# Kernel optimization log

Hardware: AMD Instinct MI355X
Metric: run time of the kernel (lower is better)

## Reference

```python
import jax, jax.numpy as jnp
import numpy as np

NEG_SLOPE = 0.2

def gat_conv(x, src, dst, W, a_src, a_dst, b, num_nodes):
    # x: [N, in]; W: [in, H*F]; a_src/a_dst: [H, F]; b: [H*F]
    H, F = a_src.shape
    feat = (x @ W).reshape(-1, H, F)                 # [N, H, F]
    el = jnp.sum(feat * a_src, axis=-1)              # [N, H]
    er = jnp.sum(feat * a_dst, axis=-1)              # [N, H]
    e = jax.nn.leaky_relu(el[src] + er[dst], NEG_SLOPE)  # [E, H]
    # segment softmax over incoming edges of each dst node
    emax = jax.ops.segment_max(e, dst, num_segments=num_nodes)  # [N, H]
    ee = jnp.exp(e - emax[dst])
    denom = jax.ops.segment_sum(ee, dst, num_segments=num_nodes)  # [N, H]
    alpha = ee / denom[dst]                          # [E, H]
    msg = feat[src] * alpha[..., None]               # [E, H, F]
    out = jax.ops.segment_sum(msg, dst, num_segments=num_nodes)  # [N, H, F]
    return out + b.reshape(1, H, F)


def setup_inputs() -> dict:
    key = jax.random.key(0)
    ks = jax.random.split(key, 16)
    N, E = 50000, 800000
    IN, HID, OUT, H = 128, 32, 32, 4
    inp = {
        'features': jax.random.normal(ks[0], (N, IN), dtype=jnp.float32),
        'edge_src': jax.random.randint(ks[1], (E,), 0, N, dtype=jnp.int32),
        'edge_dst': jax.random.randint(ks[2], (E,), 0, N, dtype=jnp.int32),
        'W1': jax.random.normal(ks[3], (IN, H * HID), dtype=jnp.float32) * 0.1,
        'a1s': jax.random.normal(ks[4], (H, HID), dtype=jnp.float32) * 0.1,
        'a1d': jax.random.normal(ks[5], (H, HID), dtype=jnp.float32) * 0.1,
        'b1': jnp.zeros((H * HID,), dtype=jnp.float32),
        'W2': jax.random.normal(ks[6], (H * HID, H * HID), dtype=jnp.float32) * 0.1,
        'a2s': jax.random.normal(ks[7], (H, HID), dtype=jnp.float32) * 0.1,
        'a2d': jax.random.normal(ks[8], (H, HID), dtype=jnp.float32) * 0.1,
        'b2': jnp.zeros((H * HID,), dtype=jnp.float32),
        'W3': jax.random.normal(ks[9], (H * HID, OUT), dtype=jnp.float32) * 0.1,
        'a3s': jax.random.normal(ks[10], (1, OUT), dtype=jnp.float32) * 0.1,
        'a3d': jax.random.normal(ks[11], (1, OUT), dtype=jnp.float32) * 0.1,
        'b3': jnp.zeros((OUT,), dtype=jnp.float32),
    }
    return inp


def reference(features, edge_src, edge_dst, W1, a1s, a1d, b1, W2, a2s, a2d, b2, W3, a3s, a3d, b3):
    N = features.shape[0]
    # dropout=0.0 -> identity
    x = gat_conv(features, edge_src, edge_dst, W1, a1s, a1d, b1, N).reshape(N, -1)
    x = jax.nn.elu(x)
    x = gat_conv(x, edge_src, edge_dst, W2, a2s, a2d, b2, N).reshape(N, -1)
    x = jax.nn.elu(x)
    x = gat_conv(x, edge_src, edge_dst, W3, a3s, a3d, b3, N).mean(axis=1)  # [N, out]
    return x
```

## Files before the change

### kernel.cpp

```cpp
#include <hip/hip_runtime.h>
#include <hip/hip_fp16.h>

#define NEG_SLOPE 0.2f

typedef unsigned int uint;
typedef unsigned short ushort;
typedef __attribute__((ext_vector_type(8))) short bf16x8;
typedef __attribute__((ext_vector_type(4))) float f32x4;
typedef __attribute__((ext_vector_type(2))) float f32x2;

__device__ __forceinline__ uint pack_bf16x2(float a, float b) {
    uint ba = __float_as_uint(a);
    uint bb = __float_as_uint(b);
    uint ra = (ba + 0x7FFFu + ((ba >> 16) & 1u)) >> 16;
    uint rb = (bb + 0x7FFFu + ((bb >> 16) & 1u)) >> 16;
    return ra | (rb << 16);
}

__device__ __forceinline__ ushort bf16_rne(float v) {
    uint b = __float_as_uint(v);
    return (ushort)((b + 0x7FFFu + ((b >> 16) & 1u)) >> 16);
}

__device__ __forceinline__ f32x2 unpack2(uint u) {
    f32x2 r;
    r.x = __uint_as_float(u << 16);
    r.y = __uint_as_float(u & 0xFFFF0000u);
    return r;
}

__device__ __forceinline__ uint pack_sw(int s, float w) {
    return ((uint)s << 16) | (uint)__half_as_ushort(__float2half_rn(w));
}

__device__ __forceinline__ int sw_src(uint u) { return (int)(u >> 16); }
__device__ __forceinline__ float sw_w(uint u) {
    return __half2float(__ushort_as_half((ushort)(u & 0xFFFFu)));
}


__global__ void zero_ints(int* __restrict__ p, int n) {
    int i = blockIdx.x * 256 + threadIdx.x;
    if (i < n) p[i] = 0;
}

__global__ void hist_kernel(const int* __restrict__ dst, int* __restrict__ deg,
                            int* __restrict__ rank, int E) {
    int i = blockIdx.x * 256 + threadIdx.x;
    if (i < E) rank[i] = atomicAdd(&deg[dst[i]], 1);
}

#define SCAN_CH 2048

__global__ __launch_bounds__(256) void scan_blocksum(const int* __restrict__ deg,
                                                     int* __restrict__ bsum, int N) {
    int blk = blockIdx.x, t = threadIdx.x;
    int base = blk * SCAN_CH;
    int s = 0;
#pragma unroll
    for (int i = 0; i < SCAN_CH / 256; ++i) {
        int idx = base + t + i * 256;
        if (idx < N) s += deg[idx];
    }
#pragma unroll
    for (int off = 1; off < 64; off <<= 1) s += __shfl_xor(s, off);
    __shared__ int wt[4];
    if ((t & 63) == 0) wt[t >> 6] = s;
    __syncthreads();
    if (t == 0) bsum[blk] = wt[0] + wt[1] + wt[2] + wt[3];
}

__global__ void scan_bsum(const int* __restrict__ bsum, int* __restrict__ boff, int nb) {
    int t = threadIdx.x;
    int orig = (t < nb) ? bsum[t] : 0;
    int v = orig;
#pragma unroll
    for (int off = 1; off < 64; off <<= 1) {
        int u = __shfl_up(v, off);
        if (t >= off) v += u;
    }
    if (t < nb) boff[t] = v - orig;
}

__global__ __launch_bounds__(256) void scan_write(const int* __restrict__ deg,
                                                  const int* __restrict__ boff,
                                                  int* __restrict__ rowptr, int N) {
    int blk = blockIdx.x, t = threadIdx.x;
    int base = blk * SCAN_CH + t * 8;
    int v[8];
    int s = 0;
#pragma unroll
    for (int r = 0; r < 8; ++r) {
        int idx = base + r;
        v[r] = (idx < N) ? deg[idx] : 0;
        s += v[r];
    }
    int lane = t & 63, wid = t >> 6;
    int p = s;
#pragma unroll
    for (int off = 1; off < 64; off <<= 1) {
        int u = __shfl_up(p, off);
        if (lane >= off) p += u;
    }
    __shared__ int wtot[4];
    if (lane == 63) wtot[wid] = p;
    __syncthreads();
    int run = boff[blk];
    for (int w = 0; w < wid; ++w) run += wtot[w];
    run += p - s;
#pragma unroll
    for (int r = 0; r < 8; ++r) {
        int idx = base + r;
        if (idx < N) {
            rowptr[idx] = run;
            run += v[r];
            if (idx == N - 1) rowptr[N] = run;
        }
    }
}

__global__ void fill_kernel(const int* __restrict__ src, const int* __restrict__ dst,
                            const int* __restrict__ rowptr, const int* __restrict__ rank,
                            int* __restrict__ csrc, int E) {
    int i = blockIdx.x * 256 + threadIdx.x;
    if (i < E) {
        int d = dst[i];
        __builtin_nontemporal_store(src[i], csrc + rowptr[d] + rank[i]);
    }
}


__global__ __launch_bounds__(256) void cvt_bf16_kernel(const float* __restrict__ X,
                                                       ushort* __restrict__ Xb, int n8) {
    int i = blockIdx.x * 256 + threadIdx.x;
    if (i >= n8) return;
    const float4* xp = (const float4*)X + (size_t)i * 2;
    float4 v0 = xp[0], v1 = xp[1];
    uint4 q;
    q.x = pack_bf16x2(v0.x, v0.y);
    q.y = pack_bf16x2(v0.z, v0.w);
    q.z = pack_bf16x2(v1.x, v1.y);
    q.w = pack_bf16x2(v1.z, v1.w);
    ((uint4*)Xb)[i] = q;
}


template <int OUTF>
__global__ __launch_bounds__(256) void wpack_kernel(const float* __restrict__ W,
                                                    ushort* __restrict__ wfrag) {
    constexpr int TOT = (OUTF / 16) * 4 * 64;
    int idx = blockIdx.x * 256 + threadIdx.x;
    if (idx >= TOT) return;
    int lane = idx & 63;
    int kt = (idx >> 6) & 3;
    int ct = idx >> 8;
    int col = ct * 16 + (lane & 15);
    int k0 = kt * 32 + (lane >> 4) * 8;
    uint4 q;
    q.x = pack_bf16x2(W[(k0 + 0) * OUTF + col], W[(k0 + 1) * OUTF + col]);
    q.y = pack_bf16x2(W[(k0 + 2) * OUTF + col], W[(k0 + 3) * OUTF + col]);
    q.z = pack_bf16x2(W[(k0 + 4) * OUTF + col], W[(k0 + 5) * OUTF + col]);
    q.w = pack_bf16x2(W[(k0 + 6) * OUTF + col], W[(k0 + 7) * OUTF + col]);
    ((uint4*)wfrag)[idx] = q;
}


template <int OUTF>
__global__ __launch_bounds__(256) void gemm_mfma_kernel(const ushort* __restrict__ Xb,
                                                        const ushort* __restrict__ wfrag,
                                                        ushort* __restrict__ Yb,
                                                        const float* __restrict__ as_,
                                                        const float* __restrict__ ad_,
                                                        float* __restrict__ el,
                                                        float* __restrict__ er, int N) {
    constexpr int H = OUTF / 32;
    constexpr int NCT = OUTF / 16;
    int lane = threadIdx.x & 63;
    int wv = threadIdx.x >> 6;
    int r0 = blockIdx.x * 64 + wv * 16;
    if (r0 >= N) return;
    int lrow = lane & 15;
    int lk8 = lane >> 4;

    bf16x8 afrag[4];
    {
        int arow = min(r0 + lrow, N - 1);
        const ushort* xr = Xb + (size_t)arow * 128;
#pragma unroll
        for (int kt = 0; kt < 4; ++kt)
            afrag[kt] = *(const bf16x8*)(xr + kt * 32 + lk8 * 8);
    }

    float pel[H][4];
    float prr[H][4];
#pragma unroll
    for (int h = 0; h < H; ++h)
#pragma unroll
        for (int j = 0; j < 4; ++j) { pel[h][j] = 0.f; prr[h][j] = 0.f; }

    const bf16x8* wf = (const bf16x8*)wfrag;
#pragma unroll
    for (int ct = 0; ct < NCT; ++ct) {
        f32x4 acc = {0.f, 0.f, 0.f, 0.f};
#pragma unroll
        for (int kt = 0; kt < 4; ++kt) {
            bf16x8 b = wf[(ct * 4 + kt) * 64 + lane];
            acc = __builtin_amdgcn_mfma_f32_16x16x32_bf16(afrag[kt], b, acc, 0, 0, 0);
        }
        int col = ct * 16 + lrow;
        int h = (H == 1) ? 0 : (ct >> 1);
        float asc = as_[col], adc = ad_[col];
#pragma unroll
        for (int j = 0; j < 4; ++j) {
            int row = r0 + lk8 * 4 + j;
            float v = acc[j];
            if (row < N) Yb[(size_t)row * OUTF + col] = bf16_rne(v);
            pel[h][j] = fmaf(v, asc, pel[h][j]);
            prr[h][j] = fmaf(v, adc, prr[h][j]);
        }
    }

#pragma unroll
    for (int h = 0; h < H; ++h)
#pragma unroll
        for (int j = 0; j < 4; ++j) {
            float pe = pel[h][j], pr = prr[h][j];
#pragma unroll
            for (int off = 1; off < 16; off <<= 1) {
                pe += __shfl_xor(pe, off);
                pr += __shfl_xor(pr, off);
            }
            if (lrow == 0) {
                int row = r0 + lk8 * 4 + j;
                if (row < N) {
                    el[row * H + h] = pe;
                    er[row * H + h] = pr;
                }
            }
        }
}


template <bool DOELU>
__global__ __launch_bounds__(256) void agg4_kernel(const ushort* __restrict__ featb,
                                                   const float* __restrict__ el,
                                                   const float* __restrict__ er,
                                                   const int* __restrict__ rowptr,
                                                   const int* __restrict__ csrc,
                                                   const float* __restrict__ bias,
                                                   ushort* __restrict__ outb, int N) {
    int lane = threadIdx.x & 63;
    int node = blockIdx.x * 4 + (threadIdx.x >> 6);
    if (node >= N) return;
    int row0 = __builtin_amdgcn_readfirstlane(rowptr[node]);
    int row1 = __builtin_amdgcn_readfirstlane(rowptr[node + 1]);

    int qe = lane >> 2;
    int qh = lane & 3;
    float ern = er[node * 4 + qh];

    int g = lane >> 4;
    int li = lane & 15;
    int h = li >> 2;
    int ib = (g << 4) + (h << 2);

    float dacc = 0.f;
    f32x2 acc2[4];
#pragma unroll
    for (int r = 0; r < 4; ++r) acc2[r] = (f32x2){0.f, 0.f};

    for (int base = row0; base < row1; base += 16) {
        int e = base + qe;
        uint u = 0;
        if (e < row1) {
            int s = csrc[e];
            float tt = el[s * 4 + qh] + ern;
            tt = tt > 0.f ? tt : NEG_SLOPE * tt;
            float w = __expf(tt);
            dacc += w;
            u = pack_sw(s, w);
        }
        uint u0 = (uint)__builtin_amdgcn_ds_bpermute(ib, (int)u);
        uint u1 = (uint)__builtin_amdgcn_ds_bpermute(ib + 64, (int)u);
        uint u2 = (uint)__builtin_amdgcn_ds_bpermute(ib + 128, (int)u);
        uint u3 = (uint)__builtin_amdgcn_ds_bpermute(ib + 192, (int)u);
        uint4 U0 = *(const uint4*)(featb + (size_t)sw_src(u0) * 128 + li * 8);
        uint4 U1 = *(const uint4*)(featb + (size_t)sw_src(u1) * 128 + li * 8);
        uint4 U2 = *(const uint4*)(featb + (size_t)sw_src(u2) * 128 + li * 8);
        uint4 U3 = *(const uint4*)(featb + (size_t)sw_src(u3) * 128 + li * 8);
        float w0 = sw_w(u0), w1 = sw_w(u1), w2 = sw_w(u2), w3 = sw_w(u3);
        acc2[0] = unpack2(U0.x) * w0 + acc2[0];
        acc2[1] = unpack2(U0.y) * w0 + acc2[1];
        acc2[2] = unpack2(U0.z) * w0 + acc2[2];
        acc2[3] = unpack2(U0.w) * w0 + acc2[3];
        acc2[0] = unpack2(U1.x) * w1 + acc2[0];
        acc2[1] = unpack2(U1.y) * w1 + acc2[1];
        acc2[2] = unpack2(U1.z) * w1 + acc2[2];
        acc2[3] = unpack2(U1.w) * w1 + acc2[3];
        acc2[0] = unpack2(U2.x) * w2 + acc2[0];
        acc2[1] = unpack2(U2.y) * w2 + acc2[1];
        acc2[2] = unpack2(U2.z) * w2 + acc2[2];
        acc2[3] = unpack2(U2.w) * w2 + acc2[3];
        acc2[0] = unpack2(U3.x) * w3 + acc2[0];
        acc2[1] = unpack2(U3.y) * w3 + acc2[1];
        acc2[2] = unpack2(U3.z) * w3 + acc2[2];
        acc2[3] = unpack2(U3.w) * w3 + acc2[3];
    }

#pragma unroll
    for (int r = 0; r < 4; ++r) {
        acc2[r].x += __shfl_xor(acc2[r].x, 16);
        acc2[r].y += __shfl_xor(acc2[r].y, 16);
        acc2[r].x += __shfl_xor(acc2[r].x, 32);
        acc2[r].y += __shfl_xor(acc2[r].y, 32);
    }
#pragma unroll
    for (int off = 4; off < 64; off <<= 1) dacc += __shfl_xor(dacc, off);
    float d = __int_as_float(
        __builtin_amdgcn_ds_bpermute((li >> 2) << 2, __float_as_int(dacc)));

    if (lane < 16) {
        float inv = (row1 > row0) ? 1.f / d : 0.f;
        const float4* bv = (const float4*)bias + li * 2;
        float4 b0 = bv[0], b1 = bv[1];
        float o[8];
        o[0] = acc2[0].x * inv + b0.x;
        o[1] = acc2[0].y * inv + b0.y;
        o[2] = acc2[1].x * inv + b0.z;
        o[3] = acc2[1].y * inv + b0.w;
        o[4] = acc2[2].x * inv + b1.x;
        o[5] = acc2[2].y * inv + b1.y;
        o[6] = acc2[3].x * inv + b1.z;
        o[7] = acc2[3].y * inv + b1.w;
        if (DOELU) {
#pragma unroll
            for (int r = 0; r < 8; ++r) o[r] = o[r] > 0.f ? o[r] : __expf(o[r]) - 1.f;
        }
        uint4 q;
        q.x = pack_bf16x2(o[0], o[1]);
        q.y = pack_bf16x2(o[2], o[3]);
        q.z = pack_bf16x2(o[4], o[5]);
        q.w = pack_bf16x2(o[6], o[7]);
        *(uint4*)(outb + (size_t)node * 128 + li * 8) = q;
    }
}


__global__ __launch_bounds__(256) void agg1_kernel(const ushort* __restrict__ featb,
                                                   const float* __restrict__ el,
                                                   const float* __restrict__ er,
                                                   const int* __restrict__ rowptr,
                                                   const int* __restrict__ csrc,
                                                   const float* __restrict__ bias,
                                                   float* __restrict__ out, int N) {
    int lane = threadIdx.x & 63;
    int node = blockIdx.x * 4 + (threadIdx.x >> 6);
    if (node >= N) return;
    int row0 = __builtin_amdgcn_readfirstlane(rowptr[node]);
    int row1 = __builtin_amdgcn_readfirstlane(rowptr[node + 1]);

    float ern = er[node];
    int g = lane >> 3;
    int li = lane & 7;

    float dacc = 0.f;
    f32x2 acc2[2];
    acc2[0] = (f32x2){0.f, 0.f};
    acc2[1] = (f32x2){0.f, 0.f};

    for (int base = row0; base < row1; base += 64) {
        int e = base + lane;
        uint u = 0;
        if (e < row1) {
            int s = csrc[e];
            float t0 = el[s] + ern;
            t0 = t0 > 0.f ? t0 : NEG_SLOPE * t0;
            float w0 = __expf(t0);
            dacc += w0;
            u = pack_sw(s, w0);
        }
        int cnt = min(row1 - base, 64);
        int iters = (cnt + 7) >> 3;
        int it = 0;
        for (; it + 1 < iters; it += 2) {
            int idxA = ((it << 3) + g) << 2;
            int idxB = (((it + 1) << 3) + g) << 2;
            uint uA = (uint)__builtin_amdgcn_ds_bpermute(idxA, (int)u);
            uint uB = (uint)__builtin_amdgcn_ds_bpermute(idxB, (int)u);
            uint2 UA = *(const uint2*)(featb + (size_t)sw_src(uA) * 32 + li * 4);
            uint2 UB = *(const uint2*)(featb + (size_t)sw_src(uB) * 32 + li * 4);
            float wA = sw_w(uA), wB = sw_w(uB);
            acc2[0] = unpack2(UA.x) * wA + acc2[0];
            acc2[1] = unpack2(UA.y) * wA + acc2[1];
            acc2[0] = unpack2(UB.x) * wB + acc2[0];
            acc2[1] = unpack2(UB.y) * wB + acc2[1];
        }
        if (it < iters) {
            int idx = ((it << 3) + g) << 2;
            uint uS = (uint)__builtin_amdgcn_ds_bpermute(idx, (int)u);
            uint2 U = *(const uint2*)(featb + (size_t)sw_src(uS) * 32 + li * 4);
            float wS = sw_w(uS);
            acc2[0] = unpack2(U.x) * wS + acc2[0];
            acc2[1] = unpack2(U.y) * wS + acc2[1];
        }
    }

#pragma unroll
    for (int r = 0; r < 2; ++r) {
        acc2[r].x += __shfl_xor(acc2[r].x, 8);
        acc2[r].y += __shfl_xor(acc2[r].y, 8);
        acc2[r].x += __shfl_xor(acc2[r].x, 16);
        acc2[r].y += __shfl_xor(acc2[r].y, 16);
        acc2[r].x += __shfl_xor(acc2[r].x, 32);
        acc2[r].y += __shfl_xor(acc2[r].y, 32);
    }
#pragma unroll
    for (int off = 1; off < 64; off <<= 1) dacc += __shfl_xor(dacc, off);

    if (lane < 8) {
        float inv = (row1 > row0) ? 1.f / dacc : 0.f;
        float4 b0 = ((const float4*)bias)[lane];
        float4 q;
        q.x = acc2[0].x * inv + b0.x;
        q.y = acc2[0].y * inv + b0.y;
        q.z = acc2[1].x * inv + b0.z;
        q.w = acc2[1].y * inv + b0.w;
        ((float4*)(out + (size_t)node * 32))[lane] = q;
    }
}


extern "C" void kernel_launch(void* const* d_in, const int* in_sizes, int n_in,
                              void* d_out, int out_size, void* d_ws, size_t ws_size,
                              hipStream_t stream) {
    const float* features = (const float*)d_in[0];
    const int* esrc = (const int*)d_in[1];
    const int* edst = (const int*)d_in[2];
    const float* W1 = (const float*)d_in[3];
    const float* a1s = (const float*)d_in[4];
    const float* a1d = (const float*)d_in[5];
    const float* b1 = (const float*)d_in[6];
    const float* W2 = (const float*)d_in[7];
    const float* a2s = (const float*)d_in[8];
    const float* a2d = (const float*)d_in[9];
    const float* b2 = (const float*)d_in[10];
    const float* W3 = (const float*)d_in[11];
    const float* a3s = (const float*)d_in[12];
    const float* a3d = (const float*)d_in[13];
    const float* b3 = (const float*)d_in[14];

    int N = in_sizes[0] / 128;
    int E = in_sizes[1];
    int nb = (N + SCAN_CH - 1) / SCAN_CH;

    char* base = (char*)d_ws;
    size_t off = 0;
    auto nxt = [&](size_t bytes) {
        void* p = base + off;
        off += (bytes + 255) & ~(size_t)255;
        return p;
    };
    ushort* Xb = (ushort*)nxt((size_t)N * 128 * 2);
    ushort* Yb = (ushort*)nxt((size_t)N * 128 * 2);
    ushort* Bb = (ushort*)nxt((size_t)N * 128 * 2);
    ushort* Y3b = (ushort*)nxt((size_t)N * 32 * 2);
    float* el = (float*)nxt((size_t)N * 4 * 4);
    float* er = (float*)nxt((size_t)N * 4 * 4);
    int* deg = (int*)nxt((size_t)N * 4);
    int* rowptr = (int*)nxt((size_t)(N + 1) * 4);
    int* csrc = (int*)nxt((size_t)E * 4);
    int* rank = (int*)nxt((size_t)E * 4);
    int* bsum = (int*)nxt((size_t)(nb + 1) * 4);
    int* boff = (int*)nxt((size_t)(nb + 1) * 4);
    ushort* wf1 = (ushort*)nxt(16384 * 2);
    ushort* wf2 = (ushort*)nxt(16384 * 2);
    ushort* wf3 = (ushort*)nxt(4096 * 2);

    int gemm_grid = (N + 63) / 64;

    zero_ints<<<(N + 255) / 256, 256, 0, stream>>>(deg, N);
    hist_kernel<<<(E + 255) / 256, 256, 0, stream>>>(edst, deg, rank, E);
    cvt_bf16_kernel<<<(N * 16 + 255) / 256, 256, 0, stream>>>(features, Xb, N * 16);
    wpack_kernel<128><<<8, 256, 0, stream>>>(W1, wf1);
    wpack_kernel<128><<<8, 256, 0, stream>>>(W2, wf2);
    wpack_kernel<32><<<2, 256, 0, stream>>>(W3, wf3);
    scan_blocksum<<<nb, 256, 0, stream>>>(deg, bsum, N);
    scan_bsum<<<1, 64, 0, stream>>>(bsum, boff, nb);
    scan_write<<<nb, 256, 0, stream>>>(deg, boff, rowptr, N);
    fill_kernel<<<(E + 255) / 256, 256, 0, stream>>>(esrc, edst, rowptr, rank, csrc, E);

    gemm_mfma_kernel<128><<<gemm_grid, 256, 0, stream>>>(Xb, wf1, Yb, a1s, a1d, el, er, N);
    agg4_kernel<true><<<(N + 3) / 4, 256, 0, stream>>>(Yb, el, er, rowptr, csrc, b1, Bb, N);

    gemm_mfma_kernel<128><<<gemm_grid, 256, 0, stream>>>(Bb, wf2, Yb, a2s, a2d, el, er, N);
    agg4_kernel<true><<<(N + 3) / 4, 256, 0, stream>>>(Yb, el, er, rowptr, csrc, b2, Bb, N);

    gemm_mfma_kernel<32><<<gemm_grid, 256, 0, stream>>>(Bb, wf3, Y3b, a3s, a3d, el, er, N);
    agg1_kernel<<<(N + 3) / 4, 256, 0, stream>>>(Y3b, el, er, rowptr, csrc, b3,
                                                 (float*)d_out, N);
}
```

Measured before the change: 225.7 us.

## Merge prep kernels, use memset for degree zeroing, prefetch next edge in agg4

The bf16 feature conversion and the three weight-packing kernels become one prep kernel that dispatches on block index, and the degree-zeroing kernel becomes a hipMemsetAsync. Together these cut several small launches from the preprocessing chain. The agg4 aggregation loop now loads the next chunk's source index and el value before the current chunk's gathers and FMAs, hiding some of the dependent load latency. The prefetch keeps extra values live in registers and adds loads on the last iteration.

```diff
diff --git a/kernel.cpp b/kernel.cpp
--- a/kernel.cpp
+++ b/kernel.cpp
@@ -38,11 +38,6 @@
     return __half2float(__ushort_as_half((ushort)(u & 0xFFFFu)));
 }
 
-
-__global__ void zero_ints(int* __restrict__ p, int n) {
-    int i = blockIdx.x * 256 + threadIdx.x;
-    if (i < n) p[i] = 0;
-}
 
 __global__ void hist_kernel(const int* __restrict__ dst, int* __restrict__ deg,
                             int* __restrict__ rank, int E) {
@@ -130,26 +125,10 @@
 }
 
 
-__global__ __launch_bounds__(256) void cvt_bf16_kernel(const float* __restrict__ X,
-                                                       ushort* __restrict__ Xb, int n8) {
-    int i = blockIdx.x * 256 + threadIdx.x;
-    if (i >= n8) return;
-    const float4* xp = (const float4*)X + (size_t)i * 2;
-    float4 v0 = xp[0], v1 = xp[1];
-    uint4 q;
-    q.x = pack_bf16x2(v0.x, v0.y);
-    q.y = pack_bf16x2(v0.z, v0.w);
-    q.z = pack_bf16x2(v1.x, v1.y);
-    q.w = pack_bf16x2(v1.z, v1.w);
-    ((uint4*)Xb)[i] = q;
-}
-
-
 template <int OUTF>
-__global__ __launch_bounds__(256) void wpack_kernel(const float* __restrict__ W,
-                                                    ushort* __restrict__ wfrag) {
+__device__ __forceinline__ void wpack_body(const float* __restrict__ W,
+                                           ushort* __restrict__ wfrag, int idx) {
     constexpr int TOT = (OUTF / 16) * 4 * 64;
-    int idx = blockIdx.x * 256 + threadIdx.x;
     if (idx >= TOT) return;
     int lane = idx & 63;
     int kt = (idx >> 6) & 3;
@@ -162,6 +141,37 @@
     q.z = pack_bf16x2(W[(k0 + 4) * OUTF + col], W[(k0 + 5) * OUTF + col]);
     q.w = pack_bf16x2(W[(k0 + 6) * OUTF + col], W[(k0 + 7) * OUTF + col]);
     ((uint4*)wfrag)[idx] = q;
+}
+
+__global__ __launch_bounds__(256) void prep_kernel(const float* __restrict__ X,
+                                                   ushort* __restrict__ Xb, int n8,
+                                                   int cvtblocks,
+                                                   const float* __restrict__ W1,
+                                                   ushort* __restrict__ wf1,
+                                                   const float* __restrict__ W2,
+                                                   ushort* __restrict__ wf2,
+                                                   const float* __restrict__ W3,
+                                                   ushort* __restrict__ wf3) {
+    int b = blockIdx.x;
+    int t = threadIdx.x;
+    if (b < cvtblocks) {
+        int i = b * 256 + t;
+        if (i >= n8) return;
+        const float4* xp = (const float4*)X + (size_t)i * 2;
+        float4 v0 = xp[0], v1 = xp[1];
+        uint4 q;
+        q.x = pack_bf16x2(v0.x, v0.y);
+        q.y = pack_bf16x2(v0.z, v0.w);
+        q.z = pack_bf16x2(v1.x, v1.y);
+        q.w = pack_bf16x2(v1.z, v1.w);
+        ((uint4*)Xb)[i] = q;
+    } else if (b < cvtblocks + 8) {
+        wpack_body<128>(W1, wf1, (b - cvtblocks) * 256 + t);
+    } else if (b < cvtblocks + 16) {
+        wpack_body<128>(W2, wf2, (b - cvtblocks - 8) * 256 + t);
+    } else {
+        wpack_body<32>(W3, wf3, (b - cvtblocks - 16) * 256 + t);
+    }
 }
 
 
@@ -269,17 +279,25 @@
 #pragma unroll
     for (int r = 0; r < 4; ++r) acc2[r] = (f32x2){0.f, 0.f};
 
+    int e0 = row0 + qe;
+    bool v = e0 < row1;
+    int s = v ? csrc[e0] : 0;
+    float elv = v ? el[s * 4 + qh] : 0.f;
+
     for (int base = row0; base < row1; base += 16) {
-        int e = base + qe;
         uint u = 0;
-        if (e < row1) {
-            int s = csrc[e];
-            float tt = el[s * 4 + qh] + ern;
+        if (v) {
+            float tt = elv + ern;
             tt = tt > 0.f ? tt : NEG_SLOPE * tt;
             float w = __expf(tt);
             dacc += w;
             u = pack_sw(s, w);
         }
+        int en = base + 16 + qe;
+        bool vn = en < row1;
+        int sn = vn ? csrc[en] : 0;
+        float elvn = vn ? el[sn * 4 + qh] : 0.f;
+
         uint u0 = (uint)__builtin_amdgcn_ds_bpermute(ib, (int)u);
         uint u1 = (uint)__builtin_amdgcn_ds_bpermute(ib + 64, (int)u);
         uint u2 = (uint)__builtin_amdgcn_ds_bpermute(ib + 128, (int)u);
@@ -305,6 +323,8 @@
         acc2[1] = unpack2(U3.y) * w3 + acc2[1];
         acc2[2] = unpack2(U3.z) * w3 + acc2[2];
         acc2[3] = unpack2(U3.w) * w3 + acc2[3];
+
+        v = vn; s = sn; elv = elvn;
     }
 
 #pragma unroll
@@ -477,13 +497,13 @@
     ushort* wf3 = (ushort*)nxt(4096 * 2);
 
     int gemm_grid = (N + 63) / 64;
-
-    zero_ints<<<(N + 255) / 256, 256, 0, stream>>>(deg, N);
+    int n8 = N * 16;
+    int cvtblocks = (n8 + 255) / 256;
+
+    hipMemsetAsync(deg, 0, (size_t)N * 4, stream);
     hist_kernel<<<(E + 255) / 256, 256, 0, stream>>>(edst, deg, rank, E);
-    cvt_bf16_kernel<<<(N * 16 + 255) / 256, 256, 0, stream>>>(features, Xb, N * 16);
-    wpack_kernel<128><<<8, 256, 0, stream>>>(W1, wf1);
-    wpack_kernel<128><<<8, 256, 0, stream>>>(W2, wf2);
-    wpack_kernel<32><<<2, 256, 0, stream>>>(W3, wf3);
+    prep_kernel<<<cvtblocks + 18, 256, 0, stream>>>(features, Xb, n8, cvtblocks,
+                                                    W1, wf1, W2, wf2, W3, wf3);
     scan_blocksum<<<nb, 256, 0, stream>>>(deg, bsum, N);
     scan_bsum<<<1, 64, 0, stream>>>(bsum, boff, nb);
     scan_write<<<nb, 256, 0, stream>>>(deg, boff, rowptr, N);
```

Result: faster. 218.7 us (-3.1%).
